# Optimization experiments

Measured on AMD Instinct MI355X. Metric: run time of the kernel, lower is better.

The kernel has to match this reference:

```python
import jax, jax.numpy as jnp
import numpy as np

# ---- static configuration (from SSN.configure) ----
B, H, W = 2, 512, 512
N_SV = 1024
Kh = int(np.floor(np.sqrt(float(N_SV) * H / W)))  # 32
Kw = int(np.floor(np.sqrt(float(N_SV) * W / H)))  # 32
K = Kh * Kw                                       # 1024
P_SCALE = 0.4
LAB_SCALE = 0.26
SOFTSCALE = -1.0
NUM_STEPS = 5
YX_SCALE = max(Kh / (P_SCALE * H), Kw / (P_SCALE * W))
INVALID_DIST = 1e10


def setup_inputs() -> dict:
    key = jax.random.key(0)
    img_lab = jax.random.normal(key, (B, 3, H, W), dtype=jnp.float32)
    # regular-grid initial superpixel index, as SSN initializes it
    ys = (jnp.arange(H, dtype=jnp.int32) * Kh) // H   # (H,) in [0,Kh)
    xs = (jnp.arange(W, dtype=jnp.int32) * Kw) // W   # (W,) in [0,Kw)
    init = ys[:, None] * Kw + xs[None, :]             # (H,W) in [0,K)
    init_spIndx = jnp.broadcast_to(init, (B, H, W))
    return {"img_lab": img_lab, "init_spIndx": init_spIndx}


def _pfeat_yxlab(img_lab):
    # (B,5,H,W): scaled Y, X positions + scaled LAB color
    Y = jnp.broadcast_to(jnp.arange(H, dtype=img_lab.dtype)[None, None, :, None], (B, 1, H, W))
    X = jnp.broadcast_to(jnp.arange(W, dtype=img_lab.dtype)[None, None, None, :], (B, 1, H, W))
    return jnp.concatenate([YX_SCALE * Y, YX_SCALE * X, LAB_SCALE * img_lab], axis=1)


def _neighbor_indices(init_spIndx):
    # 3x3 superpixel-grid neighborhood of each pixel's init superpixel
    ki = init_spIndx // Kw  # (B,H,W)
    kj = init_spIndx % Kw
    offs = jnp.array([(di, dj) for di in (-1, 0, 1) for dj in (-1, 0, 1)], dtype=jnp.int32)  # (9,2)
    ni = ki[:, None] + offs[:, 0][None, :, None, None]  # (B,9,H,W)
    nj = kj[:, None] + offs[:, 1][None, :, None, None]
    valid = (ni >= 0) & (ni < Kh) & (nj >= 0) & (nj < Kw)
    idx = jnp.clip(ni, 0, Kh - 1) * Kw + jnp.clip(nj, 0, Kw - 1)  # (B,9,H,W) in [0,K)
    return idx, valid


def _seg_sum(vals, idx):
    # vals (B, C, N), idx (B, N) -> (B, C, K)
    return jax.vmap(lambda v, i: jax.ops.segment_sum(v.T, i, num_segments=K).T)(vals, idx)


def _sp_feat_gather(pFeat, init_spIndx):
    # spFeatGather2d: per-superpixel mean of pixel features -> (B,C,K)
    C = pFeat.shape[1]
    pf = pFeat.reshape(B, C, H * W)
    ix = init_spIndx.reshape(B, H * W)
    fsum = _seg_sum(pf, ix)
    cnt = jax.vmap(lambda i: jax.ops.segment_sum(jnp.ones((H * W,), jnp.float32), i, num_segments=K))(ix)
    return fsum / jnp.maximum(cnt, 1.0)[:, None, :]


def _psp_assoc(pFeat, spFeat, idx, valid):
    # softmax over 9 local superpixels of scaled squared distance
    nbr = jax.vmap(lambda sf, ix: sf[:, ix])(spFeat, idx)          # (B,C,9,H,W)
    dist = jnp.sum((pFeat[:, :, None] - nbr) ** 2, axis=1)          # (B,9,H,W)
    dist = jnp.where(valid, dist, INVALID_DIST)
    return jax.nn.softmax(SOFTSCALE * dist, axis=1)


def _sp_feat_update(pFeat, assoc, idx, valid):
    # spFeatUpdate2d: association-weighted scatter-mean into superpixels
    C = pFeat.shape[1]
    w = jnp.where(valid, assoc, 0.0)                                # (B,9,H,W)
    contrib = (pFeat[:, :, None] * w[:, None]).reshape(B, C, 9 * H * W)
    flat_i = idx.reshape(B, 9 * H * W)
    fsum = _seg_sum(contrib, flat_i)                                # (B,C,K)
    wsum = jax.vmap(lambda wv, i: jax.ops.segment_sum(wv, i, num_segments=K))(w.reshape(B, -1), flat_i)
    return fsum / jnp.maximum(wsum, 1e-10)[:, None, :]


def reference(img_lab, init_spIndx):
    pFeat = _pfeat_yxlab(img_lab)                      # (B,5,H,W)
    idx, valid = _neighbor_indices(init_spIndx)        # (B,9,H,W)
    spFeat = _sp_feat_gather(pFeat, init_spIndx)       # (B,5,K)
    for _ in range(1, NUM_STEPS):
        assoc = _psp_assoc(pFeat, spFeat, idx, valid)
        spFeat = _sp_feat_update(pFeat, assoc, idx, valid)
    psp_assoc = _psp_assoc(pFeat, spFeat, idx, valid)  # (B,9,H,W)
    rel = jnp.argmax(psp_assoc, axis=1)                # (B,H,W)
    final_spIndx = jnp.take_along_axis(idx, rel[:, None], axis=1)[:, 0]  # (B,H,W)
    return pFeat, spFeat, psp_assoc, final_spIndx
```

## Files before the change

kernel.cpp:

```cpp
#include <hip/hip_runtime.h>

namespace {
constexpr int B = 2, H = 512, W = 512;
constexpr int KH = 32, KW = 32, K = 1024;
constexpr int HW = H * W;
constexpr float YX_SCALE = 0.15625f;
constexpr float LAB_SCALE = 0.26f;
}

template <int CTRL>
__device__ __forceinline__ float dpp_add(float v) {
  int r = __builtin_amdgcn_update_dpp(0, __float_as_int(v), CTRL, 0xF, 0xF, true);
  return v + __int_as_float(r);
}
__device__ __forceinline__ float wave_sum64(float v) {
  v = dpp_add<0xB1>(v);
  v = dpp_add<0x4E>(v);
  v = dpp_add<0x141>(v);
  v = dpp_add<0x140>(v);
  v = dpp_add<0x142>(v);
  v = dpp_add<0x143>(v);
  return v;
}

__global__ __launch_bounds__(256) void ssn_init(const float* __restrict__ lab,
                                                float* __restrict__ outPFeat,
                                                float* __restrict__ partial) {
  const int cell = blockIdx.x;
  const int b = cell >> 10;
  const int k = cell & (K - 1);
  const int ki = k >> 5, kj = k & 31;
  const int t = threadIdx.x;
  const int y = (ki << 4) + (t >> 4);
  const int x = (kj << 4) + (t & 15);
  const int pix = y * W + x;
  const float* labB = lab + (size_t)b * 3 * HW;

  float f[5];
  f[0] = YX_SCALE * (float)y;
  f[1] = YX_SCALE * (float)x;
  f[2] = LAB_SCALE * labB[pix];
  f[3] = LAB_SCALE * labB[HW + pix];
  f[4] = LAB_SCALE * labB[2 * HW + pix];

  float* po = outPFeat + (size_t)b * 5 * HW + pix;
#pragma unroll
  for (int c = 0; c < 5; ++c) po[(size_t)c * HW] = f[c];

  if (t < 54 && (t < 24 || t >= 30)) partial[(size_t)cell * 54 + t] = 0.0f;

  float s[5];
#pragma unroll
  for (int c = 0; c < 5; ++c) s[c] = wave_sum64(f[c]);
  __shared__ float red[4][5];
  if ((t & 63) == 63) {
#pragma unroll
    for (int c = 0; c < 5; ++c) red[t >> 6][c] = s[c];
  }
  __syncthreads();
  if (t < 5)
    partial[(size_t)cell * 54 + 25 + t] = red[0][t] + red[1][t] + red[2][t] + red[3][t];
  if (t == 5)
    partial[(size_t)cell * 54 + 24] = 256.0f;
}

__global__ __launch_bounds__(256) void ssn_update(const float* __restrict__ lab,
                                                  const float* __restrict__ pin,
                                                  float* __restrict__ pout) {
  __shared__ float sfl[4][54];
  const int lane = threadIdx.x & 63;
  const int wid = threadIdx.x >> 6;
  const int cell = blockIdx.x * 4 + wid;
  const int b = cell >> 10;
  const int k = cell & (K - 1);
  const int ki = k >> 5, kj = k & 31;

  float gsum = 0.0f;
  if (lane < 54) {
    const int n = lane / 6, comp = lane % 6;
    const int nki = ki + n / 3 - 1, nkj = kj + n % 3 - 1;
    if ((unsigned)nki < (unsigned)KH && (unsigned)nkj < (unsigned)KW) {
#pragma unroll
      for (int j = 0; j < 9; ++j) {
        const int ci = nki - (j / 3 - 1), cj = nkj - (j % 3 - 1);
        if ((unsigned)ci < (unsigned)KH && (unsigned)cj < (unsigned)KW)
          gsum += pin[(size_t)((b << 10) + (ci << 5) + cj) * 54 + j * 6 + comp];
      }
    }
    sfl[wid][lane] = gsum;
  }
  __syncthreads();

  float sf[9][5];
  bool valid[9];
#pragma unroll
  for (int n = 0; n < 9; ++n) {
    const int ni = ki + n / 3 - 1, nj = kj + n % 3 - 1;
    valid[n] = ((unsigned)ni < (unsigned)KH) && ((unsigned)nj < (unsigned)KW);
    const float inv = 1.0f / fmaxf(sfl[wid][n * 6], 1e-10f);
#pragma unroll
    for (int c = 0; c < 5; ++c) sf[n][c] = sfl[wid][n * 6 + 1 + c] * inv;
  }

  float acc[54];
#pragma unroll
  for (int i = 0; i < 54; ++i) acc[i] = 0.0f;

  const float* labB = lab + (size_t)b * 3 * HW;
#pragma unroll
  for (int px = 0; px < 4; ++px) {
    const int t = lane + px * 64;
    const int y = (ki << 4) + (t >> 4);
    const int x = (kj << 4) + (t & 15);
    const int pix = y * W + x;
    float f[5];
    f[0] = YX_SCALE * (float)y;
    f[1] = YX_SCALE * (float)x;
    f[2] = LAB_SCALE * labB[pix];
    f[3] = LAB_SCALE * labB[HW + pix];
    f[4] = LAB_SCALE * labB[2 * HW + pix];

    float d[9];
#pragma unroll
    for (int j = 0; j < 9; ++j) {
      float t0 = f[0] - sf[j][0];
      float dd = t0 * t0;
#pragma unroll
      for (int c = 1; c < 5; ++c) {
        const float tc = f[c] - sf[j][c];
        dd = fmaf(tc, tc, dd);
      }
      d[j] = dd;
    }
    float m = 1e30f;
#pragma unroll
    for (int j = 0; j < 9; ++j)
      if (valid[j]) m = fminf(m, d[j]);
    float e[9], sum = 0.0f;
#pragma unroll
    for (int j = 0; j < 9; ++j) {
      e[j] = valid[j] ? __expf(m - d[j]) : 0.0f;
      sum += e[j];
    }
    const float inv = 1.0f / sum;
#pragma unroll
    for (int j = 0; j < 9; ++j) {
      const float w = e[j] * inv;
      acc[j * 6 + 0] += w;
#pragma unroll
      for (int c = 0; c < 5; ++c)
        acc[j * 6 + 1 + c] = fmaf(w, f[c], acc[j * 6 + 1 + c]);
    }
  }

#pragma unroll
  for (int i = 0; i < 54; ++i) acc[i] = wave_sum64(acc[i]);
  if (lane == 63) {
    float* p = pout + (size_t)cell * 54;
#pragma unroll
    for (int i = 0; i < 54; ++i) p[i] = acc[i];
  }
}

__global__ __launch_bounds__(256) void ssn_final(const float* __restrict__ lab,
                                                 const float* __restrict__ pin,
                                                 float* __restrict__ outSpFeat,
                                                 float* __restrict__ outAssoc,
                                                 float* __restrict__ outIdx) {
  __shared__ float sfl[4][54];
  const int lane = threadIdx.x & 63;
  const int wid = threadIdx.x >> 6;
  const int cell = blockIdx.x * 4 + wid;
  const int b = cell >> 10;
  const int k = cell & (K - 1);
  const int ki = k >> 5, kj = k & 31;

  float gsum = 0.0f;
  if (lane < 54) {
    const int n = lane / 6, comp = lane % 6;
    const int nki = ki + n / 3 - 1, nkj = kj + n % 3 - 1;
    if ((unsigned)nki < (unsigned)KH && (unsigned)nkj < (unsigned)KW) {
#pragma unroll
      for (int j = 0; j < 9; ++j) {
        const int ci = nki - (j / 3 - 1), cj = nkj - (j % 3 - 1);
        if ((unsigned)ci < (unsigned)KH && (unsigned)cj < (unsigned)KW)
          gsum += pin[(size_t)((b << 10) + (ci << 5) + cj) * 54 + j * 6 + comp];
      }
    }
    sfl[wid][lane] = gsum;
  }
  __syncthreads();

  if (lane == 0) {
    const float inv4 = 1.0f / fmaxf(sfl[wid][24], 1e-10f);
#pragma unroll
    for (int c = 0; c < 5; ++c)
      outSpFeat[((size_t)b * 5 + c) * K + k] = sfl[wid][25 + c] * inv4;
  }

  float sf[9][5];
  bool valid[9];
#pragma unroll
  for (int n = 0; n < 9; ++n) {
    const int ni = ki + n / 3 - 1, nj = kj + n % 3 - 1;
    valid[n] = ((unsigned)ni < (unsigned)KH) && ((unsigned)nj < (unsigned)KW);
    const float inv = 1.0f / fmaxf(sfl[wid][n * 6], 1e-10f);
#pragma unroll
    for (int c = 0; c < 5; ++c) sf[n][c] = sfl[wid][n * 6 + 1 + c] * inv;
  }

  const float* labB = lab + (size_t)b * 3 * HW;
#pragma unroll
  for (int px = 0; px < 4; ++px) {
    const int t = lane + px * 64;
    const int y = (ki << 4) + (t >> 4);
    const int x = (kj << 4) + (t & 15);
    const int pix = y * W + x;
    float f[5];
    f[0] = YX_SCALE * (float)y;
    f[1] = YX_SCALE * (float)x;
    f[2] = LAB_SCALE * labB[pix];
    f[3] = LAB_SCALE * labB[HW + pix];
    f[4] = LAB_SCALE * labB[2 * HW + pix];

    float d[9];
#pragma unroll
    for (int j = 0; j < 9; ++j) {
      float t0 = f[0] - sf[j][0];
      float dd = t0 * t0;
#pragma unroll
      for (int c = 1; c < 5; ++c) {
        const float tc = f[c] - sf[j][c];
        dd = fmaf(tc, tc, dd);
      }
      d[j] = dd;
    }
    float m = 1e30f;
#pragma unroll
    for (int j = 0; j < 9; ++j)
      if (valid[j]) m = fminf(m, d[j]);
    float e[9], sum = 0.0f;
#pragma unroll
    for (int j = 0; j < 9; ++j) {
      e[j] = valid[j] ? __expf(m - d[j]) : 0.0f;
      sum += e[j];
    }
    const float inv = 1.0f / sum;

    float* oa = outAssoc + (size_t)b * 9 * HW + pix;
#pragma unroll
    for (int j = 0; j < 9; ++j) oa[(size_t)j * HW] = e[j] * inv;

    int bestj = 4;
    float bestd = 1e30f;
#pragma unroll
    for (int j = 0; j < 9; ++j)
      if (valid[j] && d[j] < bestd) { bestd = d[j]; bestj = j; }
    const int bi = ki + bestj / 3 - 1;
    const int bj = kj + bestj % 3 - 1;
    outIdx[(size_t)b * HW + pix] = (float)(bi * KW + bj);
  }
}

extern "C" void kernel_launch(void* const* d_in, const int* in_sizes, int n_in,
                              void* d_out, int out_size, void* d_ws, size_t ws_size,
                              hipStream_t stream) {
  const float* lab = (const float*)d_in[0];

  float* out = (float*)d_out;
  float* outPFeat = out;
  float* outSpFeat = outPFeat + 2621440;
  float* outAssoc = outSpFeat + 10240;
  float* outIdx = outAssoc + 4718592;

  float* pA = (float*)d_ws;
  float* pB = pA + (size_t)B * K * 54;

  ssn_init<<<B * K, 256, 0, stream>>>(lab, outPFeat, pA);
  ssn_update<<<B * K / 4, 256, 0, stream>>>(lab, pA, pB);
  ssn_update<<<B * K / 4, 256, 0, stream>>>(lab, pB, pA);
  ssn_update<<<B * K / 4, 256, 0, stream>>>(lab, pA, pB);
  ssn_update<<<B * K / 4, 256, 0, stream>>>(lab, pB, pA);
  ssn_final<<<B * K / 4, 256, 0, stream>>>(lab, pA, outSpFeat, outAssoc, outIdx);
}
```

Baseline: 114.7 us.

## Fuse all SSN iterations into one persistent kernel with grid barriers

Replaces the init, four update and final launches with a single persistent kernel of 256 blocks. Each wave handles two superpixel cells and keeps its LAB pixel values in registers across iterations, with software grid barriers on atomic counters between phases. This removes the per-launch overhead and the repeated LAB reloads, and switches some reciprocals to the fast hardware rcp. In exchange, only 256 blocks run, which lowers parallelism and latency hiding. The spin barrier also depends on all blocks being co-resident and has a timeout break that could silently give wrong results.

```diff
diff --git a/kernel.cpp b/kernel.cpp
--- a/kernel.cpp
+++ b/kernel.cpp
@@ -4,6 +4,7 @@
 constexpr int B = 2, H = 512, W = 512;
 constexpr int KH = 32, KW = 32, K = 1024;
 constexpr int HW = H * W;
+constexpr int NBLOCKS = 256;
 constexpr float YX_SCALE = 0.15625f;
 constexpr float LAB_SCALE = 0.26f;
 }
@@ -23,242 +24,267 @@
   return v;
 }
 
-__global__ __launch_bounds__(256) void ssn_init(const float* __restrict__ lab,
-                                                float* __restrict__ outPFeat,
-                                                float* __restrict__ partial) {
-  const int cell = blockIdx.x;
-  const int b = cell >> 10;
-  const int k = cell & (K - 1);
-  const int ki = k >> 5, kj = k & 31;
-  const int t = threadIdx.x;
-  const int y = (ki << 4) + (t >> 4);
-  const int x = (kj << 4) + (t & 15);
-  const int pix = y * W + x;
-  const float* labB = lab + (size_t)b * 3 * HW;
-
-  float f[5];
-  f[0] = YX_SCALE * (float)y;
-  f[1] = YX_SCALE * (float)x;
-  f[2] = LAB_SCALE * labB[pix];
-  f[3] = LAB_SCALE * labB[HW + pix];
-  f[4] = LAB_SCALE * labB[2 * HW + pix];
-
-  float* po = outPFeat + (size_t)b * 5 * HW + pix;
-#pragma unroll
-  for (int c = 0; c < 5; ++c) po[(size_t)c * HW] = f[c];
-
-  if (t < 54 && (t < 24 || t >= 30)) partial[(size_t)cell * 54 + t] = 0.0f;
-
-  float s[5];
-#pragma unroll
-  for (int c = 0; c < 5; ++c) s[c] = wave_sum64(f[c]);
-  __shared__ float red[4][5];
-  if ((t & 63) == 63) {
-#pragma unroll
-    for (int c = 0; c < 5; ++c) red[t >> 6][c] = s[c];
-  }
+__device__ __forceinline__ float fast_rcp(float x) { return __builtin_amdgcn_rcpf(x); }
+
+__device__ __forceinline__ float gather54(const float* __restrict__ pin,
+                                          int b, int ki, int kj, int lane) {
+  float g = 0.0f;
+  const int n = lane / 6, comp = lane % 6;
+  const int nki = ki + n / 3 - 1, nkj = kj + n % 3 - 1;
+  if ((unsigned)nki < (unsigned)KH && (unsigned)nkj < (unsigned)KW) {
+#pragma unroll
+    for (int j = 0; j < 9; ++j) {
+      const int ci = nki - (j / 3 - 1), cj = nkj - (j % 3 - 1);
+      if ((unsigned)ci < (unsigned)KH && (unsigned)cj < (unsigned)KW)
+        g += pin[(size_t)((b << 10) + (ci << 5) + cj) * 54 + j * 6 + comp];
+    }
+  }
+  return g;
+}
+
+__device__ __forceinline__ void grid_barrier(unsigned* __restrict__ ctr, int idx) {
   __syncthreads();
-  if (t < 5)
-    partial[(size_t)cell * 54 + 25 + t] = red[0][t] + red[1][t] + red[2][t] + red[3][t];
-  if (t == 5)
-    partial[(size_t)cell * 54 + 24] = 256.0f;
-}
-
-__global__ __launch_bounds__(256) void ssn_update(const float* __restrict__ lab,
-                                                  const float* __restrict__ pin,
-                                                  float* __restrict__ pout) {
-  __shared__ float sfl[4][54];
+  if (threadIdx.x == 0) {
+    __threadfence();
+    atomicAdd(&ctr[idx], 1u);
+    unsigned spins = 0;
+    while (__hip_atomic_load(&ctr[idx], __ATOMIC_ACQUIRE, __HIP_MEMORY_SCOPE_AGENT)
+           < (unsigned)NBLOCKS) {
+      __builtin_amdgcn_s_sleep(2);
+      if (++spins > 2000000u) break;
+    }
+    __threadfence();
+  }
+  __syncthreads();
+}
+
+__global__ void ssn_zero(unsigned* __restrict__ ctr) {
+  if (threadIdx.x < 8) ctr[threadIdx.x] = 0u;
+}
+
+__global__ __launch_bounds__(256) void ssn_mega(
+    const float* __restrict__ lab,
+    float* __restrict__ outPFeat, float* __restrict__ outSpFeat,
+    float* __restrict__ outAssoc, float* __restrict__ outIdx,
+    float* __restrict__ pA, float* __restrict__ pB,
+    unsigned* __restrict__ ctr) {
+  __shared__ float sfl[4][2][54];
   const int lane = threadIdx.x & 63;
   const int wid = threadIdx.x >> 6;
-  const int cell = blockIdx.x * 4 + wid;
-  const int b = cell >> 10;
-  const int k = cell & (K - 1);
-  const int ki = k >> 5, kj = k & 31;
-
-  float gsum = 0.0f;
-  if (lane < 54) {
-    const int n = lane / 6, comp = lane % 6;
-    const int nki = ki + n / 3 - 1, nkj = kj + n % 3 - 1;
-    if ((unsigned)nki < (unsigned)KH && (unsigned)nkj < (unsigned)KW) {
+  const int wg = blockIdx.x * 4 + wid;
+
+  float l0[2][4], l1[2][4], l2[2][4];
+#pragma unroll
+  for (int cc = 0; cc < 2; ++cc) {
+    const int cell = (wg << 1) + cc;
+    const int b = cell >> 10;
+    const int k = cell & (K - 1);
+    const int ki = k >> 5, kj = k & 31;
+    const float* labB = lab + (size_t)b * 3 * HW;
+    float s0 = 0, s1 = 0, s2 = 0, s3 = 0, s4 = 0;
+#pragma unroll
+    for (int px = 0; px < 4; ++px) {
+      const int t = lane + px * 64;
+      const int y = (ki << 4) + (t >> 4);
+      const int x = (kj << 4) + (t & 15);
+      const int pix = y * W + x;
+      l0[cc][px] = LAB_SCALE * labB[pix];
+      l1[cc][px] = LAB_SCALE * labB[HW + pix];
+      l2[cc][px] = LAB_SCALE * labB[2 * HW + pix];
+      const float f0 = YX_SCALE * (float)y, f1 = YX_SCALE * (float)x;
+      float* po = outPFeat + (size_t)b * 5 * HW + pix;
+      po[0] = f0;
+      po[HW] = f1;
+      po[2 * HW] = l0[cc][px];
+      po[3 * HW] = l1[cc][px];
+      po[4 * HW] = l2[cc][px];
+      s0 += f0; s1 += f1; s2 += l0[cc][px]; s3 += l1[cc][px]; s4 += l2[cc][px];
+    }
+    s0 = wave_sum64(s0); s1 = wave_sum64(s1); s2 = wave_sum64(s2);
+    s3 = wave_sum64(s3); s4 = wave_sum64(s4);
+    float* pc = pA + (size_t)cell * 54;
+    if (lane < 54 && (lane < 24 || lane > 29)) pc[lane] = 0.0f;
+    if (lane == 63) {
+      pc[24] = 256.0f;
+      pc[25] = s0; pc[26] = s1; pc[27] = s2; pc[28] = s3; pc[29] = s4;
+    }
+  }
+  grid_barrier(ctr, 0);
+
+  const float* cur = pA;
+  float* nxt = pB;
+#pragma unroll 1
+  for (int it = 0; it < 4; ++it) {
+#pragma unroll
+    for (int cc = 0; cc < 2; ++cc) {
+      const int cell = (wg << 1) + cc;
+      const int b = cell >> 10;
+      const int k = cell & (K - 1);
+      const int ki = k >> 5, kj = k & 31;
+      if (lane < 54) sfl[wid][cc][lane] = gather54(cur, b, ki, kj, lane);
+    }
+    __syncthreads();
+
+#pragma unroll
+    for (int cc = 0; cc < 2; ++cc) {
+      const int cell = (wg << 1) + cc;
+      const int b = cell >> 10;
+      const int k = cell & (K - 1);
+      const int ki = k >> 5, kj = k & 31;
+
+      float sf[9][5];
+      bool valid[9];
+#pragma unroll
+      for (int n = 0; n < 9; ++n) {
+        const int ni = ki + n / 3 - 1, nj = kj + n % 3 - 1;
+        valid[n] = ((unsigned)ni < (unsigned)KH) && ((unsigned)nj < (unsigned)KW);
+        const float inv = fast_rcp(fmaxf(sfl[wid][cc][n * 6], 1e-10f));
+#pragma unroll
+        for (int c = 0; c < 5; ++c) sf[n][c] = sfl[wid][cc][n * 6 + 1 + c] * inv;
+      }
+
+      float acc[54];
+#pragma unroll
+      for (int i = 0; i < 54; ++i) acc[i] = 0.0f;
+
+#pragma unroll
+      for (int px = 0; px < 4; ++px) {
+        const int t = lane + px * 64;
+        const int y = (ki << 4) + (t >> 4);
+        const int x = (kj << 4) + (t & 15);
+        float f[5];
+        f[0] = YX_SCALE * (float)y;
+        f[1] = YX_SCALE * (float)x;
+        f[2] = l0[cc][px]; f[3] = l1[cc][px]; f[4] = l2[cc][px];
+
+        float d[9];
+#pragma unroll
+        for (int j = 0; j < 9; ++j) {
+          float t0 = f[0] - sf[j][0];
+          float dd = t0 * t0;
+#pragma unroll
+          for (int c = 1; c < 5; ++c) {
+            const float tc = f[c] - sf[j][c];
+            dd = fmaf(tc, tc, dd);
+          }
+          d[j] = dd;
+        }
+        float m = 1e30f;
+#pragma unroll
+        for (int j = 0; j < 9; ++j)
+          if (valid[j]) m = fminf(m, d[j]);
+        float e[9], sum = 0.0f;
+#pragma unroll
+        for (int j = 0; j < 9; ++j) {
+          e[j] = valid[j] ? __expf(m - d[j]) : 0.0f;
+          sum += e[j];
+        }
+        const float inv = fast_rcp(sum);
+#pragma unroll
+        for (int j = 0; j < 9; ++j) {
+          const float w = e[j] * inv;
+          acc[j * 6 + 0] += w;
+#pragma unroll
+          for (int c = 0; c < 5; ++c)
+            acc[j * 6 + 1 + c] = fmaf(w, f[c], acc[j * 6 + 1 + c]);
+        }
+      }
+
+#pragma unroll
+      for (int i = 0; i < 54; ++i) acc[i] = wave_sum64(acc[i]);
+      if (lane == 63) {
+        float* p = nxt + (size_t)cell * 54;
+#pragma unroll
+        for (int i = 0; i < 54; ++i) p[i] = acc[i];
+      }
+    }
+    grid_barrier(ctr, 1 + it);
+    const float* tmp = cur; cur = nxt; nxt = (float*)tmp;
+  }
+
+#pragma unroll
+  for (int cc = 0; cc < 2; ++cc) {
+    const int cell = (wg << 1) + cc;
+    const int b = cell >> 10;
+    const int k = cell & (K - 1);
+    const int ki = k >> 5, kj = k & 31;
+    if (lane < 54) sfl[wid][cc][lane] = gather54(cur, b, ki, kj, lane);
+  }
+  __syncthreads();
+
+#pragma unroll
+  for (int cc = 0; cc < 2; ++cc) {
+    const int cell = (wg << 1) + cc;
+    const int b = cell >> 10;
+    const int k = cell & (K - 1);
+    const int ki = k >> 5, kj = k & 31;
+
+    if (lane == 0) {
+      const float inv4 = 1.0f / fmaxf(sfl[wid][cc][24], 1e-10f);
+#pragma unroll
+      for (int c = 0; c < 5; ++c)
+        outSpFeat[((size_t)b * 5 + c) * K + k] = sfl[wid][cc][25 + c] * inv4;
+    }
+
+    float sf[9][5];
+    bool valid[9];
+#pragma unroll
+    for (int n = 0; n < 9; ++n) {
+      const int ni = ki + n / 3 - 1, nj = kj + n % 3 - 1;
+      valid[n] = ((unsigned)ni < (unsigned)KH) && ((unsigned)nj < (unsigned)KW);
+      const float inv = 1.0f / fmaxf(sfl[wid][cc][n * 6], 1e-10f);
+#pragma unroll
+      for (int c = 0; c < 5; ++c) sf[n][c] = sfl[wid][cc][n * 6 + 1 + c] * inv;
+    }
+
+#pragma unroll
+    for (int px = 0; px < 4; ++px) {
+      const int t = lane + px * 64;
+      const int y = (ki << 4) + (t >> 4);
+      const int x = (kj << 4) + (t & 15);
+      const int pix = y * W + x;
+      float f[5];
+      f[0] = YX_SCALE * (float)y;
+      f[1] = YX_SCALE * (float)x;
+      f[2] = l0[cc][px]; f[3] = l1[cc][px]; f[4] = l2[cc][px];
+
+      float d[9];
 #pragma unroll
       for (int j = 0; j < 9; ++j) {
-        const int ci = nki - (j / 3 - 1), cj = nkj - (j % 3 - 1);
-        if ((unsigned)ci < (unsigned)KH && (unsigned)cj < (unsigned)KW)
-          gsum += pin[(size_t)((b << 10) + (ci << 5) + cj) * 54 + j * 6 + comp];
-      }
-    }
-    sfl[wid][lane] = gsum;
-  }
-  __syncthreads();
-
-  float sf[9][5];
-  bool valid[9];
-#pragma unroll
-  for (int n = 0; n < 9; ++n) {
-    const int ni = ki + n / 3 - 1, nj = kj + n % 3 - 1;
-    valid[n] = ((unsigned)ni < (unsigned)KH) && ((unsigned)nj < (unsigned)KW);
-    const float inv = 1.0f / fmaxf(sfl[wid][n * 6], 1e-10f);
-#pragma unroll
-    for (int c = 0; c < 5; ++c) sf[n][c] = sfl[wid][n * 6 + 1 + c] * inv;
-  }
-
-  float acc[54];
-#pragma unroll
-  for (int i = 0; i < 54; ++i) acc[i] = 0.0f;
-
-  const float* labB = lab + (size_t)b * 3 * HW;
-#pragma unroll
-  for (int px = 0; px < 4; ++px) {
-    const int t = lane + px * 64;
-    const int y = (ki << 4) + (t >> 4);
-    const int x = (kj << 4) + (t & 15);
-    const int pix = y * W + x;
-    float f[5];
-    f[0] = YX_SCALE * (float)y;
-    f[1] = YX_SCALE * (float)x;
-    f[2] = LAB_SCALE * labB[pix];
-    f[3] = LAB_SCALE * labB[HW + pix];
-    f[4] = LAB_SCALE * labB[2 * HW + pix];
-
-    float d[9];
-#pragma unroll
-    for (int j = 0; j < 9; ++j) {
-      float t0 = f[0] - sf[j][0];
-      float dd = t0 * t0;
-#pragma unroll
-      for (int c = 1; c < 5; ++c) {
-        const float tc = f[c] - sf[j][c];
-        dd = fmaf(tc, tc, dd);
-      }
-      d[j] = dd;
-    }
-    float m = 1e30f;
-#pragma unroll
-    for (int j = 0; j < 9; ++j)
-      if (valid[j]) m = fminf(m, d[j]);
-    float e[9], sum = 0.0f;
-#pragma unroll
-    for (int j = 0; j < 9; ++j) {
-      e[j] = valid[j] ? __expf(m - d[j]) : 0.0f;
-      sum += e[j];
-    }
-    const float inv = 1.0f / sum;
-#pragma unroll
-    for (int j = 0; j < 9; ++j) {
-      const float w = e[j] * inv;
-      acc[j * 6 + 0] += w;
-#pragma unroll
-      for (int c = 0; c < 5; ++c)
-        acc[j * 6 + 1 + c] = fmaf(w, f[c], acc[j * 6 + 1 + c]);
-    }
-  }
-
-#pragma unroll
-  for (int i = 0; i < 54; ++i) acc[i] = wave_sum64(acc[i]);
-  if (lane == 63) {
-    float* p = pout + (size_t)cell * 54;
-#pragma unroll
-    for (int i = 0; i < 54; ++i) p[i] = acc[i];
-  }
-}
-
-__global__ __launch_bounds__(256) void ssn_final(const float* __restrict__ lab,
-                                                 const float* __restrict__ pin,
-                                                 float* __restrict__ outSpFeat,
-                                                 float* __restrict__ outAssoc,
-                                                 float* __restrict__ outIdx) {
-  __shared__ float sfl[4][54];
-  const int lane = threadIdx.x & 63;
-  const int wid = threadIdx.x >> 6;
-  const int cell = blockIdx.x * 4 + wid;
-  const int b = cell >> 10;
-  const int k = cell & (K - 1);
-  const int ki = k >> 5, kj = k & 31;
-
-  float gsum = 0.0f;
-  if (lane < 54) {
-    const int n = lane / 6, comp = lane % 6;
-    const int nki = ki + n / 3 - 1, nkj = kj + n % 3 - 1;
-    if ((unsigned)nki < (unsigned)KH && (unsigned)nkj < (unsigned)KW) {
+        float t0 = f[0] - sf[j][0];
+        float dd = t0 * t0;
+#pragma unroll
+        for (int c = 1; c < 5; ++c) {
+          const float tc = f[c] - sf[j][c];
+          dd = fmaf(tc, tc, dd);
+        }
+        d[j] = dd;
+      }
+      float m = 1e30f;
+#pragma unroll
+      for (int j = 0; j < 9; ++j)
+        if (valid[j]) m = fminf(m, d[j]);
+      float e[9], sum = 0.0f;
 #pragma unroll
       for (int j = 0; j < 9; ++j) {
-        const int ci = nki - (j / 3 - 1), cj = nkj - (j % 3 - 1);
-        if ((unsigned)ci < (unsigned)KH && (unsigned)cj < (unsigned)KW)
-          gsum += pin[(size_t)((b << 10) + (ci << 5) + cj) * 54 + j * 6 + comp];
-      }
-    }
-    sfl[wid][lane] = gsum;
-  }
-  __syncthreads();
-
-  if (lane == 0) {
-    const float inv4 = 1.0f / fmaxf(sfl[wid][24], 1e-10f);
-#pragma unroll
-    for (int c = 0; c < 5; ++c)
-      outSpFeat[((size_t)b * 5 + c) * K + k] = sfl[wid][25 + c] * inv4;
-  }
-
-  float sf[9][5];
-  bool valid[9];
-#pragma unroll
-  for (int n = 0; n < 9; ++n) {
-    const int ni = ki + n / 3 - 1, nj = kj + n % 3 - 1;
-    valid[n] = ((unsigned)ni < (unsigned)KH) && ((unsigned)nj < (unsigned)KW);
-    const float inv = 1.0f / fmaxf(sfl[wid][n * 6], 1e-10f);
-#pragma unroll
-    for (int c = 0; c < 5; ++c) sf[n][c] = sfl[wid][n * 6 + 1 + c] * inv;
-  }
-
-  const float* labB = lab + (size_t)b * 3 * HW;
-#pragma unroll
-  for (int px = 0; px < 4; ++px) {
-    const int t = lane + px * 64;
-    const int y = (ki << 4) + (t >> 4);
-    const int x = (kj << 4) + (t & 15);
-    const int pix = y * W + x;
-    float f[5];
-    f[0] = YX_SCALE * (float)y;
-    f[1] = YX_SCALE * (float)x;
-    f[2] = LAB_SCALE * labB[pix];
-    f[3] = LAB_SCALE * labB[HW + pix];
-    f[4] = LAB_SCALE * labB[2 * HW + pix];
-
-    float d[9];
-#pragma unroll
-    for (int j = 0; j < 9; ++j) {
-      float t0 = f[0] - sf[j][0];
-      float dd = t0 * t0;
-#pragma unroll
-      for (int c = 1; c < 5; ++c) {
-        const float tc = f[c] - sf[j][c];
-        dd = fmaf(tc, tc, dd);
-      }
-      d[j] = dd;
-    }
-    float m = 1e30f;
-#pragma unroll
-    for (int j = 0; j < 9; ++j)
-      if (valid[j]) m = fminf(m, d[j]);
-    float e[9], sum = 0.0f;
-#pragma unroll
-    for (int j = 0; j < 9; ++j) {
-      e[j] = valid[j] ? __expf(m - d[j]) : 0.0f;
-      sum += e[j];
-    }
-    const float inv = 1.0f / sum;
-
-    float* oa = outAssoc + (size_t)b * 9 * HW + pix;
-#pragma unroll
-    for (int j = 0; j < 9; ++j) oa[(size_t)j * HW] = e[j] * inv;
-
-    int bestj = 4;
-    float bestd = 1e30f;
-#pragma unroll
-    for (int j = 0; j < 9; ++j)
-      if (valid[j] && d[j] < bestd) { bestd = d[j]; bestj = j; }
-    const int bi = ki + bestj / 3 - 1;
-    const int bj = kj + bestj % 3 - 1;
-    outIdx[(size_t)b * HW + pix] = (float)(bi * KW + bj);
+        e[j] = valid[j] ? __expf(m - d[j]) : 0.0f;
+        sum += e[j];
+      }
+      const float inv = 1.0f / sum;
+
+      float* oa = outAssoc + (size_t)b * 9 * HW + pix;
+#pragma unroll
+      for (int j = 0; j < 9; ++j) oa[(size_t)j * HW] = e[j] * inv;
+
+      int bestj = 4;
+      float bestd = 1e30f;
+#pragma unroll
+      for (int j = 0; j < 9; ++j)
+        if (valid[j] && d[j] < bestd) { bestd = d[j]; bestj = j; }
+      const int bi = ki + bestj / 3 - 1;
+      const int bj = kj + bestj % 3 - 1;
+      outIdx[(size_t)b * HW + pix] = (float)(bi * KW + bj);
+    }
   }
 }
 
@@ -275,11 +301,9 @@
 
   float* pA = (float*)d_ws;
   float* pB = pA + (size_t)B * K * 54;
-
-  ssn_init<<<B * K, 256, 0, stream>>>(lab, outPFeat, pA);
-  ssn_update<<<B * K / 4, 256, 0, stream>>>(lab, pA, pB);
-  ssn_update<<<B * K / 4, 256, 0, stream>>>(lab, pB, pA);
-  ssn_update<<<B * K / 4, 256, 0, stream>>>(lab, pA, pB);
-  ssn_update<<<B * K / 4, 256, 0, stream>>>(lab, pB, pA);
-  ssn_final<<<B * K / 4, 256, 0, stream>>>(lab, pA, outSpFeat, outAssoc, outIdx);
-}
+  unsigned* ctr = (unsigned*)(pB + (size_t)B * K * 54);
+
+  ssn_zero<<<1, 64, 0, stream>>>(ctr);
+  ssn_mega<<<NBLOCKS, 256, 0, stream>>>(lab, outPFeat, outSpFeat, outAssoc,
+                                        outIdx, pA, pB, ctr);
+}
```

New measurement: 222.1 us. 93.6% more time.

## Split superpixel cells across more waves and use fast reciprocal

Applied to the files above, without the earlier changes.

The update kernel now assigns two waves per superpixel cell instead of one, each handling half the pixels, and combines the partial 54-float sums through shared memory before writing. The final kernel uses one 256-thread block per cell with one pixel per thread, and the neighbour gather is shared by two waves rather than repeated per wave. The update path also switches to the hardware approximate reciprocal. The aim is more parallelism and shorter per-wave serial work, at the cost of an extra barrier, more blocks, and slightly different rounding.

```diff
diff --git a/kernel.cpp b/kernel.cpp
--- a/kernel.cpp
+++ b/kernel.cpp
@@ -21,6 +21,24 @@
   v = dpp_add<0x142>(v);
   v = dpp_add<0x143>(v);
   return v;
+}
+
+__device__ __forceinline__ float fast_rcp(float x) { return __builtin_amdgcn_rcpf(x); }
+
+__device__ __forceinline__ float gather54(const float* __restrict__ pin,
+                                          int b, int ki, int kj, int lane) {
+  float g = 0.0f;
+  const int n = lane / 6, comp = lane % 6;
+  const int nki = ki + n / 3 - 1, nkj = kj + n % 3 - 1;
+  if ((unsigned)nki < (unsigned)KH && (unsigned)nkj < (unsigned)KW) {
+#pragma unroll
+    for (int j = 0; j < 9; ++j) {
+      const int ci = nki - (j / 3 - 1), cj = nkj - (j % 3 - 1);
+      if ((unsigned)ci < (unsigned)KH && (unsigned)cj < (unsigned)KW)
+        g += pin[(size_t)((b << 10) + (ci << 5) + cj) * 54 + j * 6 + comp];
+    }
+  }
+  return g;
 }
 
 __global__ __launch_bounds__(256) void ssn_init(const float* __restrict__ lab,
@@ -60,34 +78,26 @@
   __syncthreads();
   if (t < 5)
     partial[(size_t)cell * 54 + 25 + t] = red[0][t] + red[1][t] + red[2][t] + red[3][t];
-  if (t == 5)
-    partial[(size_t)cell * 54 + 24] = 256.0f;
-}
-
-__global__ __launch_bounds__(256) void ssn_update(const float* __restrict__ lab,
-                                                  const float* __restrict__ pin,
-                                                  float* __restrict__ pout) {
-  __shared__ float sfl[4][54];
+  if (t == 5) partial[(size_t)cell * 54 + 24] = 256.0f;
+}
+
+__global__ __launch_bounds__(256) void ssn_update2(const float* __restrict__ lab,
+                                                   const float* __restrict__ pin,
+                                                   float* __restrict__ pout) {
+  __shared__ float sfg[2][54];
+  __shared__ float comb[2][2][54];
   const int lane = threadIdx.x & 63;
   const int wid = threadIdx.x >> 6;
-  const int cell = blockIdx.x * 4 + wid;
+  const int cidx = wid >> 1, sub = wid & 1;
+  const int cell = blockIdx.x * 2 + cidx;
   const int b = cell >> 10;
   const int k = cell & (K - 1);
   const int ki = k >> 5, kj = k & 31;
 
-  float gsum = 0.0f;
-  if (lane < 54) {
-    const int n = lane / 6, comp = lane % 6;
-    const int nki = ki + n / 3 - 1, nkj = kj + n % 3 - 1;
-    if ((unsigned)nki < (unsigned)KH && (unsigned)nkj < (unsigned)KW) {
-#pragma unroll
-      for (int j = 0; j < 9; ++j) {
-        const int ci = nki - (j / 3 - 1), cj = nkj - (j % 3 - 1);
-        if ((unsigned)ci < (unsigned)KH && (unsigned)cj < (unsigned)KW)
-          gsum += pin[(size_t)((b << 10) + (ci << 5) + cj) * 54 + j * 6 + comp];
-      }
-    }
-    sfl[wid][lane] = gsum;
+  if (wid < 2 && lane < 54) {
+    const int gcell = blockIdx.x * 2 + wid;
+    const int gk = gcell & (K - 1);
+    sfg[wid][lane] = gather54(pin, gcell >> 10, gk >> 5, gk & 31, lane);
   }
   __syncthreads();
 
@@ -97,9 +107,9 @@
   for (int n = 0; n < 9; ++n) {
     const int ni = ki + n / 3 - 1, nj = kj + n % 3 - 1;
     valid[n] = ((unsigned)ni < (unsigned)KH) && ((unsigned)nj < (unsigned)KW);
-    const float inv = 1.0f / fmaxf(sfl[wid][n * 6], 1e-10f);
-#pragma unroll
-    for (int c = 0; c < 5; ++c) sf[n][c] = sfl[wid][n * 6 + 1 + c] * inv;
+    const float inv = fast_rcp(fmaxf(sfg[cidx][n * 6], 1e-10f));
+#pragma unroll
+    for (int c = 0; c < 5; ++c) sf[n][c] = sfg[cidx][n * 6 + 1 + c] * inv;
   }
 
   float acc[54];
@@ -108,8 +118,8 @@
 
   const float* labB = lab + (size_t)b * 3 * HW;
 #pragma unroll
-  for (int px = 0; px < 4; ++px) {
-    const int t = lane + px * 64;
+  for (int pxi = 0; pxi < 2; ++pxi) {
+    const int t = lane + sub * 64 + pxi * 128;
     const int y = (ki << 4) + (t >> 4);
     const int x = (kj << 4) + (t & 15);
     const int pix = y * W + x;
@@ -142,7 +152,7 @@
       e[j] = valid[j] ? __expf(m - d[j]) : 0.0f;
       sum += e[j];
     }
-    const float inv = 1.0f / sum;
+    const float inv = fast_rcp(sum);
 #pragma unroll
     for (int j = 0; j < 9; ++j) {
       const float w = e[j] * inv;
@@ -156,46 +166,34 @@
 #pragma unroll
   for (int i = 0; i < 54; ++i) acc[i] = wave_sum64(acc[i]);
   if (lane == 63) {
-    float* p = pout + (size_t)cell * 54;
-#pragma unroll
-    for (int i = 0; i < 54; ++i) p[i] = acc[i];
-  }
-}
-
-__global__ __launch_bounds__(256) void ssn_final(const float* __restrict__ lab,
-                                                 const float* __restrict__ pin,
-                                                 float* __restrict__ outSpFeat,
-                                                 float* __restrict__ outAssoc,
-                                                 float* __restrict__ outIdx) {
-  __shared__ float sfl[4][54];
-  const int lane = threadIdx.x & 63;
-  const int wid = threadIdx.x >> 6;
-  const int cell = blockIdx.x * 4 + wid;
+#pragma unroll
+    for (int i = 0; i < 54; ++i) comb[sub][cidx][i] = acc[i];
+  }
+  __syncthreads();
+  if (wid < 2 && lane < 54) {
+    const int scell = blockIdx.x * 2 + wid;
+    pout[(size_t)scell * 54 + lane] = comb[0][wid][lane] + comb[1][wid][lane];
+  }
+}
+
+__global__ __launch_bounds__(256) void ssn_final2(const float* __restrict__ lab,
+                                                  const float* __restrict__ pin,
+                                                  float* __restrict__ outSpFeat,
+                                                  float* __restrict__ outAssoc,
+                                                  float* __restrict__ outIdx) {
+  __shared__ float sfg[54];
+  const int tid = threadIdx.x;
+  const int cell = blockIdx.x;
   const int b = cell >> 10;
   const int k = cell & (K - 1);
   const int ki = k >> 5, kj = k & 31;
 
-  float gsum = 0.0f;
-  if (lane < 54) {
-    const int n = lane / 6, comp = lane % 6;
-    const int nki = ki + n / 3 - 1, nkj = kj + n % 3 - 1;
-    if ((unsigned)nki < (unsigned)KH && (unsigned)nkj < (unsigned)KW) {
-#pragma unroll
-      for (int j = 0; j < 9; ++j) {
-        const int ci = nki - (j / 3 - 1), cj = nkj - (j % 3 - 1);
-        if ((unsigned)ci < (unsigned)KH && (unsigned)cj < (unsigned)KW)
-          gsum += pin[(size_t)((b << 10) + (ci << 5) + cj) * 54 + j * 6 + comp];
-      }
-    }
-    sfl[wid][lane] = gsum;
-  }
-  __syncthreads();
-
-  if (lane == 0) {
-    const float inv4 = 1.0f / fmaxf(sfl[wid][24], 1e-10f);
-#pragma unroll
-    for (int c = 0; c < 5; ++c)
-      outSpFeat[((size_t)b * 5 + c) * K + k] = sfl[wid][25 + c] * inv4;
+  if (tid < 54) sfg[tid] = gather54(pin, b, ki, kj, tid);
+  __syncthreads();
+
+  if (tid < 5) {
+    const float inv4 = 1.0f / fmaxf(sfg[24], 1e-10f);
+    outSpFeat[((size_t)b * 5 + tid) * K + k] = sfg[25 + tid] * inv4;
   }
 
   float sf[9][5];
@@ -204,62 +202,58 @@
   for (int n = 0; n < 9; ++n) {
     const int ni = ki + n / 3 - 1, nj = kj + n % 3 - 1;
     valid[n] = ((unsigned)ni < (unsigned)KH) && ((unsigned)nj < (unsigned)KW);
-    const float inv = 1.0f / fmaxf(sfl[wid][n * 6], 1e-10f);
-#pragma unroll
-    for (int c = 0; c < 5; ++c) sf[n][c] = sfl[wid][n * 6 + 1 + c] * inv;
-  }
-
+    const float inv = 1.0f / fmaxf(sfg[n * 6], 1e-10f);
+#pragma unroll
+    for (int c = 0; c < 5; ++c) sf[n][c] = sfg[n * 6 + 1 + c] * inv;
+  }
+
+  const int y = (ki << 4) + (tid >> 4);
+  const int x = (kj << 4) + (tid & 15);
+  const int pix = y * W + x;
   const float* labB = lab + (size_t)b * 3 * HW;
-#pragma unroll
-  for (int px = 0; px < 4; ++px) {
-    const int t = lane + px * 64;
-    const int y = (ki << 4) + (t >> 4);
-    const int x = (kj << 4) + (t & 15);
-    const int pix = y * W + x;
-    float f[5];
-    f[0] = YX_SCALE * (float)y;
-    f[1] = YX_SCALE * (float)x;
-    f[2] = LAB_SCALE * labB[pix];
-    f[3] = LAB_SCALE * labB[HW + pix];
-    f[4] = LAB_SCALE * labB[2 * HW + pix];
-
-    float d[9];
-#pragma unroll
-    for (int j = 0; j < 9; ++j) {
-      float t0 = f[0] - sf[j][0];
-      float dd = t0 * t0;
-#pragma unroll
-      for (int c = 1; c < 5; ++c) {
-        const float tc = f[c] - sf[j][c];
-        dd = fmaf(tc, tc, dd);
-      }
-      d[j] = dd;
-    }
-    float m = 1e30f;
-#pragma unroll
-    for (int j = 0; j < 9; ++j)
-      if (valid[j]) m = fminf(m, d[j]);
-    float e[9], sum = 0.0f;
-#pragma unroll
-    for (int j = 0; j < 9; ++j) {
-      e[j] = valid[j] ? __expf(m - d[j]) : 0.0f;
-      sum += e[j];
-    }
-    const float inv = 1.0f / sum;
-
-    float* oa = outAssoc + (size_t)b * 9 * HW + pix;
-#pragma unroll
-    for (int j = 0; j < 9; ++j) oa[(size_t)j * HW] = e[j] * inv;
-
-    int bestj = 4;
-    float bestd = 1e30f;
-#pragma unroll
-    for (int j = 0; j < 9; ++j)
-      if (valid[j] && d[j] < bestd) { bestd = d[j]; bestj = j; }
-    const int bi = ki + bestj / 3 - 1;
-    const int bj = kj + bestj % 3 - 1;
-    outIdx[(size_t)b * HW + pix] = (float)(bi * KW + bj);
-  }
+  float f[5];
+  f[0] = YX_SCALE * (float)y;
+  f[1] = YX_SCALE * (float)x;
+  f[2] = LAB_SCALE * labB[pix];
+  f[3] = LAB_SCALE * labB[HW + pix];
+  f[4] = LAB_SCALE * labB[2 * HW + pix];
+
+  float d[9];
+#pragma unroll
+  for (int j = 0; j < 9; ++j) {
+    float t0 = f[0] - sf[j][0];
+    float dd = t0 * t0;
+#pragma unroll
+    for (int c = 1; c < 5; ++c) {
+      const float tc = f[c] - sf[j][c];
+      dd = fmaf(tc, tc, dd);
+    }
+    d[j] = dd;
+  }
+  float m = 1e30f;
+#pragma unroll
+  for (int j = 0; j < 9; ++j)
+    if (valid[j]) m = fminf(m, d[j]);
+  float e[9], sum = 0.0f;
+#pragma unroll
+  for (int j = 0; j < 9; ++j) {
+    e[j] = valid[j] ? __expf(m - d[j]) : 0.0f;
+    sum += e[j];
+  }
+  const float inv = 1.0f / sum;
+
+  float* oa = outAssoc + (size_t)b * 9 * HW + pix;
+#pragma unroll
+  for (int j = 0; j < 9; ++j) oa[(size_t)j * HW] = e[j] * inv;
+
+  int bestj = 4;
+  float bestd = 1e30f;
+#pragma unroll
+  for (int j = 0; j < 9; ++j)
+    if (valid[j] && d[j] < bestd) { bestd = d[j]; bestj = j; }
+  const int bi = ki + bestj / 3 - 1;
+  const int bj = kj + bestj % 3 - 1;
+  outIdx[(size_t)b * HW + pix] = (float)(bi * KW + bj);
 }
 
 extern "C" void kernel_launch(void* const* d_in, const int* in_sizes, int n_in,
@@ -277,9 +271,9 @@
   float* pB = pA + (size_t)B * K * 54;
 
   ssn_init<<<B * K, 256, 0, stream>>>(lab, outPFeat, pA);
-  ssn_update<<<B * K / 4, 256, 0, stream>>>(lab, pA, pB);
-  ssn_update<<<B * K / 4, 256, 0, stream>>>(lab, pB, pA);
-  ssn_update<<<B * K / 4, 256, 0, stream>>>(lab, pA, pB);
-  ssn_update<<<B * K / 4, 256, 0, stream>>>(lab, pB, pA);
-  ssn_final<<<B * K / 4, 256, 0, stream>>>(lab, pA, outSpFeat, outAssoc, outIdx);
-}
+  ssn_update2<<<B * K / 2, 256, 0, stream>>>(lab, pA, pB);
+  ssn_update2<<<B * K / 2, 256, 0, stream>>>(lab, pB, pA);
+  ssn_update2<<<B * K / 2, 256, 0, stream>>>(lab, pA, pB);
+  ssn_update2<<<B * K / 2, 256, 0, stream>>>(lab, pB, pA);
+  ssn_final2<<<B * K, 256, 0, stream>>>(lab, pA, outSpFeat, outAssoc, outIdx);
+}
```

Measured after the change: 117.7 us. 2.7% more time.
